# Kernel tuning notes

Hardware: AMD Instinct MI355X
Metric: run time of the kernel (lower is better)

The kernel has to match this reference:

```python
import jax, jax.numpy as jnp
import numpy as np

N, NFEAT, NHID, K = 10000, 3000, 32, 10
ALPHA = 0.2


def setup_inputs() -> dict:
    key = jax.random.key(0)
    k1, k2, k3, k4, k5 = jax.random.split(key, 5)
    stdv = 1.0 / np.sqrt(NHID)
    x = jax.random.normal(k1, (N, NFEAT), dtype=jnp.float32)
    adj = jax.random.uniform(k2, (N, N), dtype=jnp.float32) / N  # row-stochastic-ish
    W = jax.random.uniform(k3, (NFEAT, NHID), minval=-stdv, maxval=stdv, dtype=jnp.float32)
    b = jax.random.uniform(k4, (NHID,), minval=-stdv, maxval=stdv, dtype=jnp.float32)
    mu = jax.random.normal(k5, (K, NHID), dtype=jnp.float32)
    return {"x": x, "adj": adj, "W": W, "b": b, "mu": mu}


def reference(x, adj, W, b, mu):
    # GCN layer: adj @ (x @ W) + b
    support = jnp.matmul(x, W)            # [N, NHID]
    z = jnp.matmul(adj, support) + b      # [N, NHID]
    # Student-t soft assignment (computed without materializing [N, K, NHID]):
    # ||z_i - mu_j||^2 = |z_i|^2 - 2 z_i.mu_j + |mu_j|^2
    z2 = jnp.sum(z * z, axis=1, keepdims=True)        # [N, 1]
    mu2 = jnp.sum(mu * mu, axis=1)                    # [K]
    d2 = z2 - 2.0 * jnp.matmul(z, mu.T) + mu2         # [N, K]
    q = 1.0 / (1.0 + d2 / ALPHA + 1e-08)
    q = q ** (ALPHA + 1.0) / 2.0
    q = q / jnp.sum(q, axis=1, keepdims=True)
    return z, q
```

## Files before the change

kernel.cpp:

```cpp
#include <hip/hip_runtime.h>
#include <math.h>


#define NH   32
#define SUBK 160
#define TRB  128

__device__ __forceinline__ void fma4k(const float4* __restrict__ bs,
                                      const float4* a, float acc[4][4])
{
#pragma unroll
    for (int t = 0; t < 4; ++t) {
        float4 b = bs[t * 8];
#pragma unroll
        for (int m = 0; m < 4; ++m) {
            float av = (t == 0) ? a[m].x : (t == 1) ? a[m].y
                     : (t == 2) ? a[m].z : a[m].w;
            acc[m][0] += av * b.x;
            acc[m][1] += av * b.y;
            acc[m][2] += av * b.z;
            acc[m][3] += av * b.w;
        }
    }
}

__global__ __launch_bounds__(256) void gemm_stream32(
    const float* __restrict__ A,
    const float* __restrict__ B,
    float* __restrict__ outp,
    int M, int K, int CH)
{
    __shared__ float Bs[SUBK * NH];

    const int tid     = threadIdx.x;
    const int rowslot = tid >> 3;
    const int jg      = tid & 7;
    const int row0    = blockIdx.x * TRB;
    const int sy      = blockIdx.y;
    const int k0      = sy * CH;
    const int kspl    = min(CH, K - k0);

    const float* ap[4];
#pragma unroll
    for (int m = 0; m < 4; ++m) {
        int r = row0 + rowslot + (m << 5);
        if (r > M - 1) r = M - 1;
        ap[m] = A + (size_t)r * K + k0;
    }

    float acc[4][4];
#pragma unroll
    for (int m = 0; m < 4; ++m)
#pragma unroll
        for (int j = 0; j < 4; ++j) acc[m][j] = 0.0f;

    for (int kb = 0; kb < kspl; kb += SUBK) {
        const int kcnt = min(SUBK, kspl - kb);

        {
            const float4* src = (const float4*)(B + (size_t)(k0 + kb) * NH);
            float4* dst = (float4*)Bs;
            for (int i = tid; i < kcnt * 8; i += 256) dst[i] = src[i];
        }
        __syncthreads();

        const float4* p0 = (const float4*)(ap[0] + kb);
        const float4* p1 = (const float4*)(ap[1] + kb);
        const float4* p2 = (const float4*)(ap[2] + kb);
        const float4* p3 = (const float4*)(ap[3] + kb);
        const float4* bs = ((const float4*)Bs) + jg;

        float4 W0[4], W1[4];
        W0[0] = p0[0]; W0[1] = p1[0]; W0[2] = p2[0]; W0[3] = p3[0];

        const int nIter = kcnt >> 3;
        for (int it = 0; it < nIter - 1; ++it) {
            W1[0] = p0[1]; W1[1] = p1[1]; W1[2] = p2[1]; W1[3] = p3[1];
            fma4k(bs, W0, acc);
            W0[0] = p0[2]; W0[1] = p1[2]; W0[2] = p2[2]; W0[3] = p3[2];
            fma4k(bs + 32, W1, acc);
            p0 += 2; p1 += 2; p2 += 2; p3 += 2;
            bs += 64;
        }
        W1[0] = p0[1]; W1[1] = p1[1]; W1[2] = p2[1]; W1[3] = p3[1];
        fma4k(bs, W0, acc);
        fma4k(bs + 32, W1, acc);

        __syncthreads();
    }

    float* op = outp + (size_t)sy * M * NH;
#pragma unroll
    for (int m = 0; m < 4; ++m) {
        int gr = row0 + rowslot + (m << 5);
        if (gr < M) {
            float4 v = make_float4(acc[m][0], acc[m][1], acc[m][2], acc[m][3]);
            *(float4*)(op + (size_t)gr * NH + (jg << 2)) = v;
        }
    }
}

__global__ __launch_bounds__(256) void reduce_add(
    const float* __restrict__ parts,
    const float* __restrict__ bias,
    float* __restrict__ out,
    int total4, int nsplit)
{
    int i = blockIdx.x * blockDim.x + threadIdx.x;
    if (i >= total4) return;
    float4 s = make_float4(0.f, 0.f, 0.f, 0.f);
    for (int p = 0; p < nsplit; ++p) {
        float4 v = ((const float4*)parts)[(size_t)p * total4 + i];
        s.x += v.x; s.y += v.y; s.z += v.z; s.w += v.w;
    }
    if (bias) {
        float4 bv = ((const float4*)bias)[i & 7];
        s.x += bv.x; s.y += bv.y; s.z += bv.z; s.w += bv.w;
    }
    ((float4*)out)[i] = s;
}

__global__ __launch_bounds__(256) void qkern(
    const float* __restrict__ z,
    const float* __restrict__ mu,
    float* __restrict__ q,
    int N)
{
    const int tid  = threadIdx.x;
    const int lane = tid & 31;
    const int i    = blockIdx.x * 8 + (tid >> 5);
    if (i >= N) return;

    float zv = z[i * 32 + lane];
    float qm = 0.f, qsum = 0.f;
#pragma unroll
    for (int c = 0; c < 10; ++c) {
        float d = zv - mu[c * 32 + lane];
        float p = d * d;
#pragma unroll
        for (int m = 16; m >= 1; m >>= 1) p += __shfl_xor(p, m, 32);
        float t  = 1.0f + p * 5.0f + 1e-8f;
        float qc = powf(t, -1.2f) * 0.5f;
        qsum += qc;
        if (lane == c) qm = qc;
    }
    if (lane < 10) q[i * 10 + lane] = qm / qsum;
}

extern "C" void kernel_launch(void* const* d_in, const int* in_sizes, int n_in,
                              void* d_out, int out_size, void* d_ws, size_t ws_size,
                              hipStream_t stream)
{
    const float* x   = (const float*)d_in[0];
    const float* adj = (const float*)d_in[1];
    const float* W   = (const float*)d_in[2];
    const float* b   = (const float*)d_in[3];
    const float* mu  = (const float*)d_in[4];

    const int N = 10000, NFEAT = 3000;
    float* z_out = (float*)d_out;
    float* q_out = (float*)d_out + N * NH;

    const size_t need32 = (size_t)(32 + 1) * N * NH * sizeof(float);
    const int nsplit = (ws_size >= need32) ? 32 : 16;

    float* ws_part    = (float*)d_ws;
    float* ws_support = (float*)d_ws + (size_t)nsplit * N * NH;

    const int total4  = N * NH / 4;
    const int rowBlks = (N + TRB - 1) / TRB;
    const int redBlks = (total4 + 255) / 256;

    const int ch1 = ((NFEAT + nsplit - 1) / nsplit + 7) & ~7;
    const int ch2 = ((N     + nsplit - 1) / nsplit + 7) & ~7;

    gemm_stream32<<<dim3(rowBlks, nsplit), 256, 0, stream>>>(
        x, W, ws_part, N, NFEAT, ch1);
    reduce_add<<<redBlks, 256, 0, stream>>>(ws_part, nullptr, ws_support, total4, nsplit);
    gemm_stream32<<<dim3(rowBlks, nsplit), 256, 0, stream>>>(
        adj, ws_support, ws_part, N, N, ch2);
    reduce_add<<<redBlks, 256, 0, stream>>>(ws_part, b, z_out, total4, nsplit);
    qkern<<<(N + 7) / 8, 256, 0, stream>>>(z_out, mu, q_out, N);
}
```

Baseline: 759.6 us.

## Halve GEMM row tile to 64 and deepen A-load prefetch pipeline

Shrinks each block's row tile from 128 to 64 rows, so each thread accumulates 2 rows instead of 4. This doubles the number of blocks and cuts per-thread register use, which should improve occupancy on the memory-bound streaming GEMMs. The inner loop now keeps four float4 segments per row in flight as a deeper software prefetch, and a peeled block handles chunk sizes that are not a multiple of 16. The trade-off is that each shared-memory B tile is reused across fewer rows, so B is loaded from global memory twice as often.

Result: no change. 747.7 us (-1.6%).

```diff
diff --git a/kernel.cpp b/kernel.cpp
--- a/kernel.cpp
+++ b/kernel.cpp
@@ -4,23 +4,21 @@
 
 #define NH   32
 #define SUBK 160
-#define TRB  128
+#define TRB  64
 
-__device__ __forceinline__ void fma4k(const float4* __restrict__ bs,
-                                      const float4* a, float acc[4][4])
+__device__ __forceinline__ void seg4(const float4* __restrict__ bs,
+                                     const float4 w0, const float4 w1,
+                                     float acc[2][4])
 {
 #pragma unroll
     for (int t = 0; t < 4; ++t) {
         float4 b = bs[t * 8];
-#pragma unroll
-        for (int m = 0; m < 4; ++m) {
-            float av = (t == 0) ? a[m].x : (t == 1) ? a[m].y
-                     : (t == 2) ? a[m].z : a[m].w;
-            acc[m][0] += av * b.x;
-            acc[m][1] += av * b.y;
-            acc[m][2] += av * b.z;
-            acc[m][3] += av * b.w;
-        }
+        float a0 = (t == 0) ? w0.x : (t == 1) ? w0.y : (t == 2) ? w0.z : w0.w;
+        float a1 = (t == 0) ? w1.x : (t == 1) ? w1.y : (t == 2) ? w1.z : w1.w;
+        acc[0][0] += a0 * b.x; acc[0][1] += a0 * b.y;
+        acc[0][2] += a0 * b.z; acc[0][3] += a0 * b.w;
+        acc[1][0] += a1 * b.x; acc[1][1] += a1 * b.y;
+        acc[1][2] += a1 * b.z; acc[1][3] += a1 * b.w;
     }
 }
 
@@ -40,22 +38,19 @@
     const int k0      = sy * CH;
     const int kspl    = min(CH, K - k0);
 
-    const float* ap[4];
+    int r0 = row0 + rowslot;       if (r0 > M - 1) r0 = M - 1;
+    int r1 = row0 + rowslot + 32;  if (r1 > M - 1) r1 = M - 1;
+    const float* ap0 = A + (size_t)r0 * K + k0;
+    const float* ap1 = A + (size_t)r1 * K + k0;
+
+    float acc[2][4];
 #pragma unroll
-    for (int m = 0; m < 4; ++m) {
-        int r = row0 + rowslot + (m << 5);
-        if (r > M - 1) r = M - 1;
-        ap[m] = A + (size_t)r * K + k0;
-    }
-
-    float acc[4][4];
-#pragma unroll
-    for (int m = 0; m < 4; ++m)
+    for (int m = 0; m < 2; ++m)
 #pragma unroll
         for (int j = 0; j < 4; ++j) acc[m][j] = 0.0f;
 
     for (int kb = 0; kb < kspl; kb += SUBK) {
-        const int kcnt = min(SUBK, kspl - kb);
+        int kcnt = min(SUBK, kspl - kb);
 
         {
             const float4* src = (const float4*)(B + (size_t)(k0 + kb) * NH);
@@ -64,37 +59,46 @@
         }
         __syncthreads();
 
-        const float4* p0 = (const float4*)(ap[0] + kb);
-        const float4* p1 = (const float4*)(ap[1] + kb);
-        const float4* p2 = (const float4*)(ap[2] + kb);
-        const float4* p3 = (const float4*)(ap[3] + kb);
+        const float4* q0 = (const float4*)(ap0 + kb);
+        const float4* q1 = (const float4*)(ap1 + kb);
         const float4* bs = ((const float4*)Bs) + jg;
 
-        float4 W0[4], W1[4];
-        W0[0] = p0[0]; W0[1] = p1[0]; W0[2] = p2[0]; W0[3] = p3[0];
+        if (kcnt & 8) {
+            float4 xa = q0[0], xb = q1[0], ya = q0[1], yb = q1[1];
+            seg4(bs,      xa, xb, acc);
+            seg4(bs + 32, ya, yb, acc);
+            q0 += 2; q1 += 2; bs += 64; kcnt -= 8;
+        }
 
-        const int nIter = kcnt >> 3;
-        for (int it = 0; it < nIter - 1; ++it) {
-            W1[0] = p0[1]; W1[1] = p1[1]; W1[2] = p2[1]; W1[3] = p3[1];
-            fma4k(bs, W0, acc);
-            W0[0] = p0[2]; W0[1] = p1[2]; W0[2] = p2[2]; W0[3] = p3[2];
-            fma4k(bs + 32, W1, acc);
-            p0 += 2; p1 += 2; p2 += 2; p3 += 2;
-            bs += 64;
+        if (kcnt) {
+            float4 w0a = q0[0], w0b = q1[0], w1a = q0[1], w1b = q1[1];
+            float4 w2a = q0[2], w2b = q1[2], w3a = q0[3], w3b = q1[3];
+            const int iters = (kcnt - 16) >> 4;
+            for (int it = 0; it < iters; ++it) {
+                seg4(bs,      w0a, w0b, acc); w0a = q0[4]; w0b = q1[4];
+                seg4(bs + 32, w1a, w1b, acc); w1a = q0[5]; w1b = q1[5];
+                seg4(bs + 64, w2a, w2b, acc); w2a = q0[6]; w2b = q1[6];
+                seg4(bs + 96, w3a, w3b, acc); w3a = q0[7]; w3b = q1[7];
+                q0 += 4; q1 += 4; bs += 128;
+            }
+            seg4(bs,      w0a, w0b, acc);
+            seg4(bs + 32, w1a, w1b, acc);
+            seg4(bs + 64, w2a, w2b, acc);
+            seg4(bs + 96, w3a, w3b, acc);
         }
-        W1[0] = p0[1]; W1[1] = p1[1]; W1[2] = p2[1]; W1[3] = p3[1];
-        fma4k(bs, W0, acc);
-        fma4k(bs + 32, W1, acc);
-
         __syncthreads();
     }
 
     float* op = outp + (size_t)sy * M * NH;
-#pragma unroll
-    for (int m = 0; m < 4; ++m) {
-        int gr = row0 + rowslot + (m << 5);
+    {
+        int gr = row0 + rowslot;
         if (gr < M) {
-            float4 v = make_float4(acc[m][0], acc[m][1], acc[m][2], acc[m][3]);
+            float4 v = make_float4(acc[0][0], acc[0][1], acc[0][2], acc[0][3]);
+            *(float4*)(op + (size_t)gr * NH + (jg << 2)) = v;
+        }
+        gr = row0 + rowslot + 32;
+        if (gr < M) {
+            float4 v = make_float4(acc[1][0], acc[1][1], acc[1][2], acc[1][3]);
             *(float4*)(op + (size_t)gr * NH + (jg << 2)) = v;
         }
     }
```
